# Kernel tuning notes

Hardware: AMD Instinct MI355X
Metric: run time of the kernel (lower is better)

The kernel has to match this reference:

```python
import jax, jax.numpy as jnp
import numpy as np

NUM_FIELDS = 39
PER_FIELD_VOCAB = 10000
TOTAL_VOCAB = NUM_FIELDS * PER_FIELD_VOCAB
EMBED_DIM = 128
DIM_INT = (2, 3)
RANKS = (128, 128)
BATCH = 2048


def setup_inputs() -> dict:
    key = jax.random.key(0)
    k_x, k_emb, k_lin, k_b, k_w0, k_w1 = jax.random.split(key, 6)
    x = jax.random.randint(k_x, (BATCH, NUM_FIELDS), 0, PER_FIELD_VOCAB, dtype=jnp.int64 if jax.config.jax_enable_x64 else jnp.int32)
    embed_table = jax.random.normal(k_emb, (TOTAL_VOCAB, EMBED_DIM), dtype=jnp.float32) * 0.01
    linear_table = jax.random.normal(k_lin, (TOTAL_VOCAB, 1), dtype=jnp.float32) * 0.01
    bias = jnp.zeros((1,), dtype=jnp.float32)
    # trunc_normal_(std=0.01) approximated by scaled normal (same distribution family)
    W0 = jax.random.normal(k_w0, (DIM_INT[0], RANKS[0], NUM_FIELDS), dtype=jnp.float32) * 0.01
    W1 = jax.random.normal(k_w1, (DIM_INT[1], RANKS[1], NUM_FIELDS), dtype=jnp.float32) * 0.01
    return {"x": x, "embed_table": embed_table, "linear_table": linear_table,
            "bias": bias, "W0": W0, "W1": W1}


def _calc_cross(emb, W):
    # emb: [B, F, D]; W: [L, R, F]
    # dot_products[b,d,r,l] = sum_f W[l,r,f] * emb[b,f,d]   (torch: 'bljk,bki->bijl')
    dp = jnp.einsum('lrf,bfd->bdrl', W, emb)          # [B, D, R, L]
    prod_over_l = jnp.prod(dp, axis=3)                # [B, D, R]
    return jnp.sum(prod_over_l, axis=(1, 2))[:, None]  # [B, 1]


def reference(x, embed_table, linear_table, bias, W0, W1):
    # per-field offsets into the flat embedding table (FeaturesEmbedding behavior)
    offsets = (jnp.arange(NUM_FIELDS) * PER_FIELD_VOCAB).astype(x.dtype)
    idx = x + offsets[None, :]                        # [B, F]
    emb = embed_table[idx]                            # [B, F, D]
    # FeaturesLinear: sum of per-feature weights + bias -> [B, 1]
    ret = jnp.sum(linear_table[idx], axis=1) + bias
    for W in (W0, W1):
        ret = ret + _calc_cross(emb, W)
    return (ret, 0)
```

## Files before the change

kernel.cpp:

```cpp
#include <hip/hip_runtime.h>
#include <hip/hip_bf16.h>

#define NUM_FIELDS 39
#define PER_FIELD_VOCAB 10000
#define EMBED_DIM 128
#define KPAD 64
#define NL 5
#define RANK 128
#define BATCH 2048

typedef __bf16  bf16x8  __attribute__((ext_vector_type(8)));
typedef float   f32x4   __attribute__((ext_vector_type(4)));

__global__ __launch_bounds__(256) void prep_w(const float* __restrict__ W0,
                                              const float* __restrict__ W1,
                                              __bf16* __restrict__ Wb) {
    int i = blockIdx.x * 256 + threadIdx.x;
    if (i >= NL * RANK * KPAD) return;
    int f = i & (KPAD - 1);
    int r = (i >> 6) & (RANK - 1);
    int l = i >> 13;
    float v = 0.f;
    if (f < NUM_FIELDS) {
        if (l < 2) v = W0[(l * RANK + r) * NUM_FIELDS + f];
        else       v = W1[((l - 2) * RANK + r) * NUM_FIELDS + f];
    }
    Wb[i] = (__bf16)v;
}

__global__ __launch_bounds__(512) void tfm_main(const int* __restrict__ x,
                                                const float* __restrict__ embed_table,
                                                const float* __restrict__ linear_table,
                                                const float* __restrict__ bias,
                                                const __bf16* __restrict__ Wb,
                                                float* __restrict__ out,
                                                int out_size) {
    __shared__ int   sidx[NUM_FIELDS];
    __shared__ __align__(16) __bf16 eT[EMBED_DIM * KPAD];
    __shared__ float wpart[8];

    const int tid = threadIdx.x;
    const int b   = blockIdx.x;

    if (tid < NUM_FIELDS)
        sidx[tid] = x[b * NUM_FIELDS + tid] + tid * PER_FIELD_VOCAB;
    __syncthreads();

    float partial = (tid < NUM_FIELDS) ? linear_table[sidx[tid]] : 0.f;

    char* eTb = (char*)eT;
#pragma unroll
    for (int it = 0; it < 2; ++it) {
        int u  = it * 512 + tid;
        int f8 = u >> 7;
        int d  = u & (EMBED_DIM - 1);
        float v[8];
#pragma unroll
        for (int j = 0; j < 8; ++j) {
            int f = f8 * 8 + j;
            v[j] = (f < NUM_FIELDS) ? embed_table[(long)sidx[f] * EMBED_DIM + d]
                                    : 0.f;
        }
        bf16x8 pk;
#pragma unroll
        for (int j = 0; j < 8; ++j) pk[j] = (__bf16)v[j];
        int off = d * 128 + ((f8 * 16) ^ ((d & 7) << 4));
        *reinterpret_cast<bf16x8*>(eTb + off) = pk;
    }
    __syncthreads();

    const int wave = tid >> 6, lane = tid & 63;
    const int m = lane & 15, quad = lane >> 4;
    const int r0 = wave * 16;

    bf16x8 afrag[NL][2];
#pragma unroll
    for (int l = 0; l < NL; ++l)
#pragma unroll
        for (int kc = 0; kc < 2; ++kc)
            afrag[l][kc] = *reinterpret_cast<const bf16x8*>(
                &Wb[(size_t)(l * RANK + r0 + m) * KPAD + kc * 32 + quad * 8]);

    f32x4 psum = {0.f, 0.f, 0.f, 0.f};

    for (int dt = 0; dt < 8; ++dt) {
        const int row = dt * 16 + m;
        bf16x8 bfrag[2];
#pragma unroll
        for (int kc = 0; kc < 2; ++kc) {
            int off = row * 128 + ((kc * 64 + quad * 16) ^ ((m & 7) << 4));
            bfrag[kc] = *reinterpret_cast<const bf16x8*>(eTb + off);
        }

        f32x4 acc[NL];
#pragma unroll
        for (int l = 0; l < NL; ++l) {
            acc[l] = (f32x4){0.f, 0.f, 0.f, 0.f};
#pragma unroll
            for (int kc = 0; kc < 2; ++kc)
                acc[l] = __builtin_amdgcn_mfma_f32_16x16x32_bf16(
                    afrag[l][kc], bfrag[kc], acc[l], 0, 0, 0);
        }
        psum += acc[0] * acc[1] + acc[2] * acc[3] * acc[4];
    }

    partial += psum[0] + psum[1] + psum[2] + psum[3];

#pragma unroll
    for (int off = 32; off > 0; off >>= 1)
        partial += __shfl_down(partial, off, 64);
    if (lane == 0) wpart[wave] = partial;
    __syncthreads();
    if (tid == 0) {
        float s = bias[0];
#pragma unroll
        for (int w = 0; w < 8; ++w) s += wpart[w];
        out[b] = s;
    }

    if (b == 0)
        for (int j = BATCH + tid; j < out_size; j += 512)
            out[j] = 0.f;
}

extern "C" void kernel_launch(void* const* d_in, const int* in_sizes, int n_in,
                              void* d_out, int out_size, void* d_ws, size_t ws_size,
                              hipStream_t stream) {
    const int*   x            = (const int*)d_in[0];
    const float* embed_table  = (const float*)d_in[1];
    const float* linear_table = (const float*)d_in[2];
    const float* bias         = (const float*)d_in[3];
    const float* W0           = (const float*)d_in[4];
    const float* W1           = (const float*)d_in[5];
    __bf16*      Wb           = (__bf16*)d_ws;

    prep_w<<<(NL * RANK * KPAD + 255) / 256, 256, 0, stream>>>(W0, W1, Wb);
    tfm_main<<<BATCH, 512, 0, stream>>>(x, embed_table, linear_table, bias, Wb,
                                        (float*)d_out, out_size);
}
```

Baseline: 287.3 us.

## Fuse weight bf16 conversion into main kernel and halve block size

```diff
diff --git a/kernel.cpp b/kernel.cpp
--- a/kernel.cpp
+++ b/kernel.cpp
@@ -11,33 +11,20 @@
 
 typedef __bf16  bf16x8  __attribute__((ext_vector_type(8)));
 typedef float   f32x4   __attribute__((ext_vector_type(4)));
+typedef float   f32x4u  __attribute__((ext_vector_type(4), aligned(4)));
+typedef float   f32x2u  __attribute__((ext_vector_type(2), aligned(4)));
 
-__global__ __launch_bounds__(256) void prep_w(const float* __restrict__ W0,
-                                              const float* __restrict__ W1,
-                                              __bf16* __restrict__ Wb) {
-    int i = blockIdx.x * 256 + threadIdx.x;
-    if (i >= NL * RANK * KPAD) return;
-    int f = i & (KPAD - 1);
-    int r = (i >> 6) & (RANK - 1);
-    int l = i >> 13;
-    float v = 0.f;
-    if (f < NUM_FIELDS) {
-        if (l < 2) v = W0[(l * RANK + r) * NUM_FIELDS + f];
-        else       v = W1[((l - 2) * RANK + r) * NUM_FIELDS + f];
-    }
-    Wb[i] = (__bf16)v;
-}
-
-__global__ __launch_bounds__(512) void tfm_main(const int* __restrict__ x,
+__global__ __launch_bounds__(256) void tfm_main(const int* __restrict__ x,
                                                 const float* __restrict__ embed_table,
                                                 const float* __restrict__ linear_table,
                                                 const float* __restrict__ bias,
-                                                const __bf16* __restrict__ Wb,
+                                                const float* __restrict__ W0,
+                                                const float* __restrict__ W1,
                                                 float* __restrict__ out,
                                                 int out_size) {
     __shared__ int   sidx[NUM_FIELDS];
     __shared__ __align__(16) __bf16 eT[EMBED_DIM * KPAD];
-    __shared__ float wpart[8];
+    __shared__ float wpart[4];
 
     const int tid = threadIdx.x;
     const int b   = blockIdx.x;
@@ -50,8 +37,8 @@
 
     char* eTb = (char*)eT;
 #pragma unroll
-    for (int it = 0; it < 2; ++it) {
-        int u  = it * 512 + tid;
+    for (int it = 0; it < 4; ++it) {
+        int u  = it * 256 + tid;
         int f8 = u >> 7;
         int d  = u & (EMBED_DIM - 1);
         float v[8];
@@ -71,37 +58,61 @@
 
     const int wave = tid >> 6, lane = tid & 63;
     const int m = lane & 15, quad = lane >> 4;
-    const int r0 = wave * 16;
-
-    bf16x8 afrag[NL][2];
-#pragma unroll
-    for (int l = 0; l < NL; ++l)
-#pragma unroll
-        for (int kc = 0; kc < 2; ++kc)
-            afrag[l][kc] = *reinterpret_cast<const bf16x8*>(
-                &Wb[(size_t)(l * RANK + r0 + m) * KPAD + kc * 32 + quad * 8]);
 
     f32x4 psum = {0.f, 0.f, 0.f, 0.f};
 
-    for (int dt = 0; dt < 8; ++dt) {
-        const int row = dt * 16 + m;
-        bf16x8 bfrag[2];
+    for (int rti = 0; rti < 2; ++rti) {
+        const int r = (wave * 2 + rti) * 16 + m;
+
+        bf16x8 afrag[NL][2];
 #pragma unroll
-        for (int kc = 0; kc < 2; ++kc) {
-            int off = row * 128 + ((kc * 64 + quad * 16) ^ ((m & 7) << 4));
-            bfrag[kc] = *reinterpret_cast<const bf16x8*>(eTb + off);
+        for (int l = 0; l < NL; ++l) {
+            const float* Wrow = (l < 2)
+                ? W0 + (size_t)(l * RANK + r) * NUM_FIELDS
+                : W1 + (size_t)((l - 2) * RANK + r) * NUM_FIELDS;
+            f32x4u wa = *reinterpret_cast<const f32x4u*>(Wrow + quad * 8);
+            f32x4u wb = *reinterpret_cast<const f32x4u*>(Wrow + quad * 8 + 4);
+            bf16x8 A0;
+#pragma unroll
+            for (int j = 0; j < 4; ++j) { A0[j] = (__bf16)wa[j]; A0[4 + j] = (__bf16)wb[j]; }
+            afrag[l][0] = A0;
+
+            bf16x8 A1;
+            if (quad == 0) {
+                f32x4u wc = *reinterpret_cast<const f32x4u*>(Wrow + 32);
+                f32x2u wd = *reinterpret_cast<const f32x2u*>(Wrow + 36);
+                float  we = Wrow[38];
+                A1[0] = (__bf16)wc[0]; A1[1] = (__bf16)wc[1];
+                A1[2] = (__bf16)wc[2]; A1[3] = (__bf16)wc[3];
+                A1[4] = (__bf16)wd[0]; A1[5] = (__bf16)wd[1];
+                A1[6] = (__bf16)we;    A1[7] = (__bf16)0.f;
+            } else {
+#pragma unroll
+                for (int j = 0; j < 8; ++j) A1[j] = (__bf16)0.f;
+            }
+            afrag[l][1] = A1;
         }
 
-        f32x4 acc[NL];
+        for (int dt = 0; dt < 8; ++dt) {
+            const int row = dt * 16 + m;
+            bf16x8 bfrag[2];
 #pragma unroll
-        for (int l = 0; l < NL; ++l) {
-            acc[l] = (f32x4){0.f, 0.f, 0.f, 0.f};
+            for (int kc = 0; kc < 2; ++kc) {
+                int off = row * 128 + ((kc * 64 + quad * 16) ^ ((m & 7) << 4));
+                bfrag[kc] = *reinterpret_cast<const bf16x8*>(eTb + off);
+            }
+
+            f32x4 acc[NL];
 #pragma unroll
-            for (int kc = 0; kc < 2; ++kc)
-                acc[l] = __builtin_amdgcn_mfma_f32_16x16x32_bf16(
-                    afrag[l][kc], bfrag[kc], acc[l], 0, 0, 0);
+            for (int l = 0; l < NL; ++l) {
+                acc[l] = (f32x4){0.f, 0.f, 0.f, 0.f};
+#pragma unroll
+                for (int kc = 0; kc < 2; ++kc)
+                    acc[l] = __builtin_amdgcn_mfma_f32_16x16x32_bf16(
+                        afrag[l][kc], bfrag[kc], acc[l], 0, 0, 0);
+            }
+            psum += acc[0] * acc[1] + acc[2] * acc[3] * acc[4];
         }
-        psum += acc[0] * acc[1] + acc[2] * acc[3] * acc[4];
     }
 
     partial += psum[0] + psum[1] + psum[2] + psum[3];
@@ -111,15 +122,11 @@
         partial += __shfl_down(partial, off, 64);
     if (lane == 0) wpart[wave] = partial;
     __syncthreads();
-    if (tid == 0) {
-        float s = bias[0];
-#pragma unroll
-        for (int w = 0; w < 8; ++w) s += wpart[w];
-        out[b] = s;
-    }
+    if (tid == 0)
+        out[b] = wpart[0] + wpart[1] + wpart[2] + wpart[3] + bias[0];
 
     if (b == 0)
-        for (int j = BATCH + tid; j < out_size; j += 512)
+        for (int j = BATCH + tid; j < out_size; j += 256)
             out[j] = 0.f;
 }
 
@@ -132,9 +139,8 @@
     const float* bias         = (const float*)d_in[3];
     const float* W0           = (const float*)d_in[4];
     const float* W1           = (const float*)d_in[5];
-    __bf16*      Wb           = (__bf16*)d_ws;
+    (void)d_ws; (void)ws_size;
 
-    prep_w<<<(NL * RANK * KPAD + 255) / 256, 256, 0, stream>>>(W0, W1, Wb);
-    tfm_main<<<BATCH, 512, 0, stream>>>(x, embed_table, linear_table, bias, Wb,
-                                        (float*)d_out, out_size);
+    tfm_main<<<BATCH, 256, 0, stream>>>(x, embed_table, linear_table, bias,
+                                        W0, W1, (float*)d_out, out_size);
 }
```

Result: slower. 361.7 us (+25.9%).
